# Optimization experiments

Measured on AMD Instinct MI355X. Metric: run time of the kernel, lower is better.

Reference implementation:

```python
import jax, jax.numpy as jnp
import numpy as np

IN_DIM, BANDS = 42, 22
H_VAD, H_NOISE, H_DEN = 24, 48, 96


def gru(x, w_ih, w_hh, b_ih, b_hh):
    """torch.nn.GRU (batch_first) semantics, h0=0.
    x: [B,T,D]; w_ih: [3H,D]; w_hh: [3H,H]; gate order r,z,n."""
    H = w_hh.shape[1]
    # precompute input projections for all timesteps (big GEMM, recurrence only on H)
    xp = jnp.einsum('btd,gd->btg', x, w_ih) + b_ih  # [B,T,3H]

    def step(h, xt):
        hp = h @ w_hh.T + b_hh
        xr, xz, xn = jnp.split(xt, 3, axis=-1)
        hr, hz, hn = jnp.split(hp, 3, axis=-1)
        r = jax.nn.sigmoid(xr + hr)
        z = jax.nn.sigmoid(xz + hz)
        n = jnp.tanh(xn + r * hn)
        h_new = (1.0 - z) * n + z * h
        return h_new, h_new

    h0 = jnp.zeros((x.shape[0], H), x.dtype)
    _, hs = jax.lax.scan(step, h0, jnp.swapaxes(xp, 0, 1))  # [T,B,H]
    return jnp.swapaxes(hs, 0, 1)  # [B,T,H]


def setup_inputs() -> dict:
    key = jax.random.key(0)
    ks = jax.random.split(key, 20)

    def w(k, shape, fan):
        return (jax.random.normal(k, shape, jnp.float32) / np.sqrt(fan)).astype(jnp.float32)

    B, T = 256, 2000
    d_noise_in = H_VAD + H_VAD + IN_DIM     # 90
    d_den_in = H_VAD + H_NOISE + IN_DIM     # 114
    return {
        'x': jax.random.normal(ks[0], (B, T, IN_DIM), jnp.float32),
        'in_w': w(ks[1], (H_VAD, IN_DIM), IN_DIM),
        'in_b': jnp.zeros((H_VAD,), jnp.float32),
        'vad_wih': w(ks[2], (3 * H_VAD, H_VAD), H_VAD),
        'vad_whh': w(ks[3], (3 * H_VAD, H_VAD), H_VAD),
        'vad_bih': jnp.zeros((3 * H_VAD,), jnp.float32),
        'vad_bhh': jnp.zeros((3 * H_VAD,), jnp.float32),
        'vad_out_w': w(ks[4], (1, H_VAD), H_VAD),
        'vad_out_b': jnp.zeros((1,), jnp.float32),
        'noise_wih': w(ks[5], (3 * H_NOISE, d_noise_in), d_noise_in),
        'noise_whh': w(ks[6], (3 * H_NOISE, H_NOISE), H_NOISE),
        'noise_bih': jnp.zeros((3 * H_NOISE,), jnp.float32),
        'noise_bhh': jnp.zeros((3 * H_NOISE,), jnp.float32),
        'den_wih': w(ks[7], (3 * H_DEN, d_den_in), d_den_in),
        'den_whh': w(ks[8], (3 * H_DEN, H_DEN), H_DEN),
        'den_bih': jnp.zeros((3 * H_DEN,), jnp.float32),
        'den_bhh': jnp.zeros((3 * H_DEN,), jnp.float32),
        'out_w': w(ks[9], (BANDS, H_DEN), H_DEN),
        'out_b': jnp.zeros((BANDS,), jnp.float32),
    }


def reference(x, in_w, in_b, vad_wih, vad_whh, vad_bih, vad_bhh,
              vad_out_w, vad_out_b, noise_wih, noise_whh, noise_bih, noise_bhh,
              den_wih, den_whh, den_bih, den_bhh, out_w, out_b):
    tmp = jnp.tanh(jnp.einsum('btd,hd->bth', x, in_w) + in_b)          # [B,T,24]
    vad_h = gru(tmp, vad_wih, vad_whh, vad_bih, vad_bhh)               # [B,T,24]
    vad = jax.nn.sigmoid(jnp.einsum('bth,oh->bto', vad_h, vad_out_w) + vad_out_b)
    noise_in = jnp.concatenate([tmp, vad_h, x], axis=-1)               # [B,T,90]
    noise_h = gru(noise_in, noise_wih, noise_whh, noise_bih, noise_bhh)  # [B,T,48]
    den_in = jnp.concatenate([vad_h, noise_h, x], axis=-1)             # [B,T,114]
    den_h = gru(den_in, den_wih, den_whh, den_bih, den_bhh)            # [B,T,96]
    gains = jax.nn.sigmoid(jnp.einsum('bth,oh->bto', den_h, out_w) + out_b)
    return gains, vad
```

## Files before the change

kernel.cpp:

```cpp
#include <hip/hip_runtime.h>

typedef _Float16 f16;
typedef _Float16 h2 __attribute__((ext_vector_type(2)));
typedef unsigned int u32;

#define TB  256
#define TTT 2000
#define INW 42
#define HV  24
#define HN  48
#define HD  96
#define NTH 640

#define DIN 0
#define DH  128
#define NIN 224
#define NH  320
#define ACTW 384

__device__ __forceinline__ float fsigm(float v) {
    return __builtin_amdgcn_rcpf(1.0f + __builtin_amdgcn_exp2f(-1.44269504089f * v));
}
__device__ __forceinline__ float ftanh(float v) {
    float e = __builtin_amdgcn_exp2f(2.88539008178f * v);
    return 1.0f - 2.0f * __builtin_amdgcn_rcpf(e + 1.0f);
}
__device__ __forceinline__ float dot2f(u32 a, u32 w, float c) {
#if __has_builtin(__builtin_amdgcn_fdot2)
    return __builtin_amdgcn_fdot2(__builtin_bit_cast(h2, a), __builtin_bit_cast(h2, w), c, false);
#else
    h2 av = __builtin_bit_cast(h2, a), wv = __builtin_bit_cast(h2, w);
    return c + (float)av[0] * (float)wv[0] + (float)av[1] * (float)wv[1];
#endif
}
__device__ __forceinline__ u32 packw(float a, float b) {
    h2 v; v[0] = (f16)a; v[1] = (f16)b;
    return __builtin_bit_cast(u32, v);
}
template<int CTRL>
__device__ __forceinline__ float dpp_add(float x) {
    int y = __builtin_amdgcn_mov_dpp(__builtin_bit_cast(int, x), CTRL, 0xF, 0xF, true);
    return x + __builtin_bit_cast(float, y);
}

#define SYNCB() asm volatile("s_waitcnt lgkmcnt(0)\n\ts_barrier" ::: "memory")

#define ACCI(AV, W, IDX) do { u32 _a = (AV); \
    rr = dot2f(_a, W[0][IDX], rr); zz = dot2f(_a, W[1][IDX], zz); an = dot2f(_a, W[2][IDX], an); } while (0)
#define ACCH(AV, W, IDX) do { u32 _a = (AV); \
    rr = dot2f(_a, W[0][IDX], rr); zz = dot2f(_a, W[1][IDX], zz); hn = dot2f(_a, W[2][IDX], hn); } while (0)
#define ACCI4(U4, W, M0) do { uint4 _u4 = (U4); \
    ACCI(_u4.x, W, (M0)+0); ACCI(_u4.y, W, (M0)+1); ACCI(_u4.z, W, (M0)+2); ACCI(_u4.w, W, (M0)+3); } while (0)
#define ACCH4(U4, W, M0) do { uint4 _u4 = (U4); \
    ACCH(_u4.x, W, (M0)+0); ACCH(_u4.y, W, (M0)+1); ACCH(_u4.z, W, (M0)+2); ACCH(_u4.w, W, (M0)+3); } while (0)
#define RED4_Q() do { \
    rr = dpp_add<0xB1>(rr); rr = dpp_add<0x4E>(rr); \
    zz = dpp_add<0xB1>(zz); zz = dpp_add<0x4E>(zz); \
    an = dpp_add<0xB1>(an); an = dpp_add<0x4E>(an); \
    hn = dpp_add<0xB1>(hn); hn = dpp_add<0x4E>(hn); } while (0)
#define RED4_1() do { \
    rr = dpp_add<0xB1>(rr); zz = dpp_add<0xB1>(zz); \
    an = dpp_add<0xB1>(an); hn = dpp_add<0xB1>(hn); } while (0)

template<int N> struct IC { static constexpr int val = N; };

__global__ __launch_bounds__(NTH, 1) void rnnoise_kernel(
    const float* __restrict__ gx,
    const float* __restrict__ in_w,      const float* __restrict__ in_b,
    const float* __restrict__ vad_wih,   const float* __restrict__ vad_whh,
    const float* __restrict__ vad_bih,   const float* __restrict__ vad_bhh,
    const float* __restrict__ vad_out_w, const float* __restrict__ vad_out_b,
    const float* __restrict__ noise_wih, const float* __restrict__ noise_whh,
    const float* __restrict__ noise_bih, const float* __restrict__ noise_bhh,
    const float* __restrict__ den_wih,   const float* __restrict__ den_whh,
    const float* __restrict__ den_bih,   const float* __restrict__ den_bhh,
    const float* __restrict__ out_w,     const float* __restrict__ out_b,
    float* __restrict__ gains, float* __restrict__ vout)
{
    __shared__ __align__(16) f16 act[8][ACTW];

    const int tid = threadIdx.x, wid = tid >> 6, lane = tid & 63;
    const int b = blockIdx.x;

    #pragma unroll
    for (int i = 0; i < 3; ++i) {
        int idx = tid + i * NTH;
        if (idx < 8 * ACTW / 2) ((u32*)act)[idx] = 0u;
    }
    __syncthreads();

    const int role = (wid == 9) ? 2 : ((wid == 4 || wid == 5 || wid == 8) ? 1 : 0);

    if (role == 0) {
        const int dwi = (wid < 4) ? wid : (wid - 2);
        const int u = 16 * dwi + (lane >> 2), q = lane & 3;
        u32 wdi[3][16], wdh[3][12];
        #pragma unroll
        for (int g = 0; g < 3; ++g) {
            const float* wi = den_wih + (g * HD + u) * 114;
            #pragma unroll
            for (int m = 0; m < 16; ++m) {
                int c = 32 * q + 2 * m;
                float a  = (c     < 114) ? wi[c]     : 0.f;
                float b2 = (c + 1 < 114) ? wi[c + 1] : 0.f;
                wdi[g][m] = packw(a, b2);
            }
            const float* wh = den_whh + (g * HD + u) * HD + 24 * q;
            #pragma unroll
            for (int m = 0; m < 12; ++m) wdh[g][m] = packw(wh[2*m], wh[2*m+1]);
        }
        const float bdr  = den_bih[u]        + den_bhh[u];
        const float bdz  = den_bih[HD + u]   + den_bhh[HD + u];
        const float bdni = den_bih[2*HD + u];
        const float bdnh = den_bhh[2*HD + u];
        float hreg = 0.f;
        float rr = 0.f, zz = 0.f, an = 0.f;

        auto step = [&](auto PC, int k) {
            constexpr int P   = decltype(PC)::val;
            constexpr int SHH = (P + 2) & 7;
            constexpr int SWR = (P + 3) & 7;
            constexpr int SB  = (P + 4) & 7;
            uint4 a0{}, a1{}, a2{}, a3{};
            if (k >= 4 && k < TTT + 4) {
                const uint4* ip = (const uint4*)&act[SB][DIN + 32 * q];
                a0 = ip[0]; a1 = ip[1]; a2 = ip[2]; a3 = ip[3];
            }
            if (k >= 5 && k < TTT + 5) {
                const uint4* hp = (const uint4*)&act[SHH][DH + 24 * q];
                uint4 h0 = hp[0], h1 = hp[1], h2 = hp[2];
                float hn = 0.f;
                ACCH4(h0, wdh, 0); ACCH4(h1, wdh, 4); ACCH4(h2, wdh, 8);
                RED4_Q();
                if (q == 0) {
                    float r = fsigm(rr + bdr);
                    float z = fsigm(zz + bdz);
                    float n = ftanh(an + bdni + r * (hn + bdnh));
                    hreg = z * (hreg - n) + n;
                    act[SWR][DH + u] = (f16)hreg;
                }
                rr = 0.f; zz = 0.f; an = 0.f;
            }
            if (k >= 4 && k < TTT + 4) {
                ACCI4(a0, wdi, 0); ACCI4(a1, wdi, 4); ACCI4(a2, wdi, 8); ACCI4(a3, wdi, 12);
            }
            SYNCB();
        };
        #pragma clang loop unroll(disable)
        for (int k0 = 0; k0 < TTT + 8; k0 += 8) {
            step(IC<0>{},k0);   step(IC<1>{},k0+1); step(IC<2>{},k0+2); step(IC<3>{},k0+3);
            step(IC<4>{},k0+4); step(IC<5>{},k0+5); step(IC<6>{},k0+6); step(IC<7>{},k0+7);
        }

    } else if (role == 1) {
        const int nwi = (wid == 4) ? 0 : ((wid == 5) ? 1 : 2);
        const int u = 16 * nwi + (lane >> 2), q = lane & 3;
        const int o = 8 * nwi + (lane >> 3), s8 = lane & 7;
        const int oc = (o < 22) ? o : 0;
        u32 wni[3][12], wnh[3][8], wo[6];
        #pragma unroll
        for (int g = 0; g < 3; ++g) {
            const float* wi = noise_wih + (g * HN + u) * 90;
            #pragma unroll
            for (int m = 0; m < 12; ++m) {
                int c = 24 * q + 2 * m;
                float a  = (c     < 90) ? wi[c]     : 0.f;
                float b2 = (c + 1 < 90) ? wi[c + 1] : 0.f;
                wni[g][m] = packw(a, b2);
            }
            const float* wh = noise_whh + (g * HN + u) * HN;
            #pragma unroll
            for (int m = 0; m < 8; ++m) {
                int c = 16 * q + 2 * m;
                float a  = (c     < 48) ? wh[c]     : 0.f;
                float b2 = (c + 1 < 48) ? wh[c + 1] : 0.f;
                wnh[g][m] = packw(a, b2);
            }
        }
        #pragma unroll
        for (int m = 0; m < 6; ++m)
            wo[m] = packw(out_w[oc*HD + 12*s8 + 2*m], out_w[oc*HD + 12*s8 + 2*m + 1]);
        const float bnr  = noise_bih[u]        + noise_bhh[u];
        const float bnz  = noise_bih[HN + u]   + noise_bhh[HN + u];
        const float bnni = noise_bih[2*HN + u];
        const float bnnh = noise_bhh[2*HN + u];
        const float bo   = out_b[oc];
        float hreg = 0.f;
        float rr = 0.f, zz = 0.f, an = 0.f;

        auto step = [&](auto PC, int k) {
            constexpr int P   = decltype(PC)::val;
            constexpr int SHH = (P + 4) & 7;
            constexpr int SWR = (P + 5) & 7;
            constexpr int SB  = (P + 6) & 7;
            constexpr int SOT = (P + 2) & 7;
            uint4 a0{}, a1{}, a2{};
            if (k >= 2 && k < TTT + 2) {
                const uint4* ip = (const uint4*)&act[SB][NIN + 24 * q];
                a0 = ip[0]; a1 = ip[1]; a2 = ip[2];
            }
            uint2 d0{}, d1{}, d2{};
            if (k >= 6 && k < TTT + 6) {
                const uint2* dp = (const uint2*)&act[SOT][DH + 12 * s8];
                d0 = dp[0]; d1 = dp[1]; d2 = dp[2];
            }
            if (k >= 3 && k < TTT + 3) {
                const uint4* hp = (const uint4*)&act[SHH][NH + 16 * q];
                uint4 h0 = hp[0], h1 = hp[1];
                float hn = 0.f;
                ACCH4(h0, wnh, 0); ACCH4(h1, wnh, 4);
                RED4_Q();
                if (q == 0) {
                    float r = fsigm(rr + bnr);
                    float z = fsigm(zz + bnz);
                    float n = ftanh(an + bnni + r * (hn + bnnh));
                    hreg = z * (hreg - n) + n;
                    f16 hh = (f16)hreg;
                    act[SWR][NH + u]       = hh;
                    act[SWR][DIN + 24 + u] = hh;
                }
                rr = 0.f; zz = 0.f; an = 0.f;
            }
            if (k >= 6 && k < TTT + 6) {
                float acc = 0;
                acc = dot2f(d0.x, wo[0], acc); acc = dot2f(d0.y, wo[1], acc);
                acc = dot2f(d1.x, wo[2], acc); acc = dot2f(d1.y, wo[3], acc);
                acc = dot2f(d2.x, wo[4], acc); acc = dot2f(d2.y, wo[5], acc);
                acc = dpp_add<0xB1>(acc); acc = dpp_add<0x4E>(acc);
                acc += __shfl_xor(acc, 4);
                if (s8 == 0 && o < 22)
                    gains[((size_t)b * TTT + (k - 6)) * 22 + o] = fsigm(acc + bo);
            }
            if (k >= 2 && k < TTT + 2) {
                ACCI4(a0, wni, 0); ACCI4(a1, wni, 4); ACCI4(a2, wni, 8);
            }
            SYNCB();
        };
        #pragma clang loop unroll(disable)
        for (int k0 = 0; k0 < TTT + 8; k0 += 8) {
            step(IC<0>{},k0);   step(IC<1>{},k0+1); step(IC<2>{},k0+2); step(IC<3>{},k0+3);
            step(IC<4>{},k0+4); step(IC<5>{},k0+5); step(IC<6>{},k0+6); step(IC<7>{},k0+7);
        }

    } else {
        const int l = lane;
        const int u = (l < 48) ? (l >> 1) : 0, q2 = l & 1;
        u32 wvi[3][6], wvh[3][6], wtm[12];
        float bvr = 0, bvz = 0, bvni = 0, bvnh = 0, btm = 0, wvo_u = 0;
        if (l < 48) {
            #pragma unroll
            for (int g = 0; g < 3; ++g) {
                const float* wi = vad_wih + (g * HV + u) * HV + 12 * q2;
                const float* wh = vad_whh + (g * HV + u) * HV + 12 * q2;
                #pragma unroll
                for (int j = 0; j < 6; ++j) {
                    wvi[g][j] = packw(wi[2*j], wi[2*j+1]);
                    wvh[g][j] = packw(wh[2*j], wh[2*j+1]);
                }
            }
            #pragma unroll
            for (int j = 0; j < 12; ++j) {
                int c0 = 24 * q2 + 2 * j;
                float a = (c0     < INW) ? in_w[u * INW + c0]     : 0.f;
                float c = (c0 + 1 < INW) ? in_w[u * INW + c0 + 1] : 0.f;
                wtm[j] = packw(a, c);
            }
            bvr  = vad_bih[u]        + vad_bhh[u];
            bvz  = vad_bih[HV + u]   + vad_bhh[HV + u];
            bvni = vad_bih[2*HV + u];
            bvnh = vad_bhh[2*HV + u];
            btm  = in_b[u];
            if (q2 == 0) wvo_u = vad_out_w[u];
        }
        const float bvo = vad_out_b[0];
        float hreg = 0.f;

        float xa = 0, xb = 0, xc = 0, xd = 0;
        if (l < INW) {
            xa = gx[((size_t)b * TTT + 0) * INW + l];
            xb = gx[((size_t)b * TTT + 1) * INW + l];
            xc = gx[((size_t)b * TTT + 2) * INW + l];
            xd = gx[((size_t)b * TTT + 3) * INW + l];
        }

        auto step = [&](auto PC, int k) {
            constexpr int P  = decltype(PC)::val;
            constexpr int ST = (P + 7) & 7;
            constexpr int SH = (P + 6) & 7;
            if (k < TTT && l < INW) {
                float xv;
                if constexpr ((P & 3) == 0) xv = xa; else if constexpr ((P & 3) == 1) xv = xb;
                else if constexpr ((P & 3) == 2) xv = xc; else xv = xd;
                f16 xh = (f16)xv;
                act[P][NIN + 48 + l] = xh;
                act[P][DIN + 72 + l] = xh;
            }
            if (k + 4 < TTT && l < INW) {
                float xv = gx[((size_t)b * TTT + (k + 4)) * INW + l];
                if constexpr ((P & 3) == 0) xa = xv; else if constexpr ((P & 3) == 1) xb = xv;
                else if constexpr ((P & 3) == 2) xc = xv; else xd = xv;
            }
            if (k >= 1 && k <= TTT) {
                float rr = 0, zz = 0, an = 0, hn = 0;
                if (l < 48) {
                    const uint2* tp = (const uint2*)&act[ST][NIN + 12 * q2];
                    const uint2* hp = (const uint2*)&act[SH][NIN + 24 + 12 * q2];
                    #pragma unroll
                    for (int v = 0; v < 3; ++v) {
                        uint2 a = tp[v]; ACCI(a.x, wvi, 2*v); ACCI(a.y, wvi, 2*v+1);
                        uint2 h = hp[v]; ACCH(h.x, wvh, 2*v); ACCH(h.y, wvh, 2*v+1);
                    }
                    RED4_1();
                    if (q2 == 0) {
                        float r = fsigm(rr + bvr);
                        float z = fsigm(zz + bvz);
                        float n = ftanh(an + bvni + r * (hn + bvnh));
                        hreg = z * (hreg - n) + n;
                        f16 hh = (f16)hreg;
                        act[ST][NIN + 24 + u] = hh;
                        act[ST][DIN + u]      = hh;
                    }
                }
                float val = (l < 48 && q2 == 0) ? (wvo_u * hreg) : 0.f;
                val = dpp_add<0xB1>(val);  val = dpp_add<0x4E>(val);
                val = dpp_add<0x124>(val); val = dpp_add<0x128>(val);
                val += __shfl_xor(val, 16); val += __shfl_xor(val, 32);
                if (l == 0) vout[(size_t)b * TTT + (k - 1)] = fsigm(val + bvo);
            }
            if (k < TTT && l < 48) {
                float acc = 0;
                const uint4* xp = (const uint4*)&act[P][NIN + 48 + 24 * q2];
                uint4 a = xp[0], b2 = xp[1], c2 = xp[2];
                acc = dot2f(a.x,  wtm[0], acc);  acc = dot2f(a.y,  wtm[1], acc);
                acc = dot2f(a.z,  wtm[2], acc);  acc = dot2f(a.w,  wtm[3], acc);
                acc = dot2f(b2.x, wtm[4], acc);  acc = dot2f(b2.y, wtm[5], acc);
                acc = dot2f(b2.z, wtm[6], acc);  acc = dot2f(b2.w, wtm[7], acc);
                acc = dot2f(c2.x, wtm[8], acc);  acc = dot2f(c2.y, wtm[9], acc);
                acc = dot2f(c2.z, wtm[10], acc); acc = dot2f(c2.w, wtm[11], acc);
                acc = dpp_add<0xB1>(acc);
                if (q2 == 0) act[P][NIN + u] = (f16)ftanh(acc + btm);
            }
            SYNCB();
        };
        #pragma clang loop unroll(disable)
        for (int k0 = 0; k0 < TTT + 8; k0 += 8) {
            step(IC<0>{},k0);   step(IC<1>{},k0+1); step(IC<2>{},k0+2); step(IC<3>{},k0+3);
            step(IC<4>{},k0+4); step(IC<5>{},k0+5); step(IC<6>{},k0+6); step(IC<7>{},k0+7);
        }
    }
}

extern "C" void kernel_launch(void* const* d_in, const int* in_sizes, int n_in,
                              void* d_out, int out_size, void* d_ws, size_t ws_size,
                              hipStream_t stream) {
    (void)in_sizes; (void)n_in; (void)d_ws; (void)ws_size; (void)out_size;
    const float* gx        = (const float*)d_in[0];
    const float* in_w      = (const float*)d_in[1];
    const float* in_b      = (const float*)d_in[2];
    const float* vad_wih   = (const float*)d_in[3];
    const float* vad_whh   = (const float*)d_in[4];
    const float* vad_bih   = (const float*)d_in[5];
    const float* vad_bhh   = (const float*)d_in[6];
    const float* vad_out_w = (const float*)d_in[7];
    const float* vad_out_b = (const float*)d_in[8];
    const float* noise_wih = (const float*)d_in[9];
    const float* noise_whh = (const float*)d_in[10];
    const float* noise_bih = (const float*)d_in[11];
    const float* noise_bhh = (const float*)d_in[12];
    const float* den_wih   = (const float*)d_in[13];
    const float* den_whh   = (const float*)d_in[14];
    const float* den_bih   = (const float*)d_in[15];
    const float* den_bhh   = (const float*)d_in[16];
    const float* out_w     = (const float*)d_in[17];
    const float* out_b     = (const float*)d_in[18];
    float* gains = (float*)d_out;
    float* vout  = (float*)d_out + (size_t)TB * (size_t)TTT * 22;

    rnnoise_kernel<<<dim3(TB), dim3(NTH), 0, stream>>>(
        gx, in_w, in_b, vad_wih, vad_whh, vad_bih, vad_bhh, vad_out_w, vad_out_b,
        noise_wih, noise_whh, noise_bih, noise_bhh, den_wih, den_whh, den_bih, den_bhh,
        out_w, out_b, gains, vout);
}
```

Before: 1.959 ms.

## Move gains output projection into denoise warps and software-pipeline input loads

Result: faster. 1.725 ms (-11.9%).

```diff
diff --git a/kernel.cpp b/kernel.cpp
--- a/kernel.cpp
+++ b/kernel.cpp
@@ -89,12 +89,15 @@
     }
     __syncthreads();
 
-    const int role = (wid == 9) ? 2 : ((wid == 4 || wid == 5 || wid == 8) ? 1 : 0);
+    const int role = (wid == 8) ? 2 : ((wid == 4 || wid == 5 || wid == 9) ? 1 : 0);
 
     if (role == 0) {
         const int dwi = (wid < 4) ? wid : (wid - 2);
         const int u = 16 * dwi + (lane >> 2), q = lane & 3;
-        u32 wdi[3][16], wdh[3][12];
+        const bool ow = (wid == 6 || wid == 7);
+        const int o = ((wid == 7) ? 11 : 0) + (lane >> 2);
+        const int oc = (ow && o < 22) ? o : 0;
+        u32 wdi[3][16], wdh[3][12], wo[12];
         #pragma unroll
         for (int g = 0; g < 3; ++g) {
             const float* wi = den_wih + (g * HD + u) * 114;
@@ -109,40 +112,50 @@
             #pragma unroll
             for (int m = 0; m < 12; ++m) wdh[g][m] = packw(wh[2*m], wh[2*m+1]);
         }
+        #pragma unroll
+        for (int m = 0; m < 12; ++m)
+            wo[m] = ow ? packw(out_w[oc*HD + 24*q + 2*m], out_w[oc*HD + 24*q + 2*m + 1]) : 0u;
         const float bdr  = den_bih[u]        + den_bhh[u];
         const float bdz  = den_bih[HD + u]   + den_bhh[HD + u];
         const float bdni = den_bih[2*HD + u];
         const float bdnh = den_bhh[2*HD + u];
+        const float bo   = ow ? out_b[oc] : 0.f;
         float hreg = 0.f;
-        float rr = 0.f, zz = 0.f, an = 0.f;
+        uint4 a0{}, a1{}, a2{}, a3{};
 
         auto step = [&](auto PC, int k) {
             constexpr int P   = decltype(PC)::val;
             constexpr int SHH = (P + 2) & 7;
             constexpr int SWR = (P + 3) & 7;
-            constexpr int SB  = (P + 4) & 7;
-            uint4 a0{}, a1{}, a2{}, a3{};
-            if (k >= 4 && k < TTT + 4) {
-                const uint4* ip = (const uint4*)&act[SB][DIN + 32 * q];
+            constexpr int SNX = (P + 4) & 7;
+            const uint4* hp = (const uint4*)&act[SHH][DH + 24 * q];
+            uint4 h0 = hp[0], h1 = hp[1], h2 = hp[2];
+            float rr = 0, zz = 0, an = 0, hn = 0;
+            ACCI4(a0, wdi, 0); ACCI4(a1, wdi, 4); ACCI4(a2, wdi, 8); ACCI4(a3, wdi, 12);
+            ACCH4(h0, wdh, 0); ACCH4(h1, wdh, 4); ACCH4(h2, wdh, 8);
+            RED4_Q();
+            if (k >= 5 && k < TTT + 5 && q == 0) {
+                float r = fsigm(rr + bdr);
+                float z = fsigm(zz + bdz);
+                float n = ftanh(an + bdni + r * (hn + bdnh));
+                hreg = z * (hreg - n) + n;
+                act[SWR][DH + u] = (f16)hreg;
+            }
+            {
+                const uint4* ip = (const uint4*)&act[SNX][DIN + 32 * q];
                 a0 = ip[0]; a1 = ip[1]; a2 = ip[2]; a3 = ip[3];
             }
-            if (k >= 5 && k < TTT + 5) {
-                const uint4* hp = (const uint4*)&act[SHH][DH + 24 * q];
-                uint4 h0 = hp[0], h1 = hp[1], h2 = hp[2];
-                float hn = 0.f;
-                ACCH4(h0, wdh, 0); ACCH4(h1, wdh, 4); ACCH4(h2, wdh, 8);
-                RED4_Q();
-                if (q == 0) {
-                    float r = fsigm(rr + bdr);
-                    float z = fsigm(zz + bdz);
-                    float n = ftanh(an + bdni + r * (hn + bdnh));
-                    hreg = z * (hreg - n) + n;
-                    act[SWR][DH + u] = (f16)hreg;
-                }
-                rr = 0.f; zz = 0.f; an = 0.f;
-            }
-            if (k >= 4 && k < TTT + 4) {
-                ACCI4(a0, wdi, 0); ACCI4(a1, wdi, 4); ACCI4(a2, wdi, 8); ACCI4(a3, wdi, 12);
+            if (ow && k >= 6 && k < TTT + 6) {
+                float acc = 0;
+                acc = dot2f(h0.x, wo[0], acc);  acc = dot2f(h0.y, wo[1], acc);
+                acc = dot2f(h0.z, wo[2], acc);  acc = dot2f(h0.w, wo[3], acc);
+                acc = dot2f(h1.x, wo[4], acc);  acc = dot2f(h1.y, wo[5], acc);
+                acc = dot2f(h1.z, wo[6], acc);  acc = dot2f(h1.w, wo[7], acc);
+                acc = dot2f(h2.x, wo[8], acc);  acc = dot2f(h2.y, wo[9], acc);
+                acc = dot2f(h2.z, wo[10], acc); acc = dot2f(h2.w, wo[11], acc);
+                acc = dpp_add<0xB1>(acc); acc = dpp_add<0x4E>(acc);
+                if (q == 0 && o < 22)
+                    gains[((size_t)b * TTT + (k - 6)) * 22 + o] = fsigm(acc + bo);
             }
             SYNCB();
         };
@@ -155,9 +168,7 @@
     } else if (role == 1) {
         const int nwi = (wid == 4) ? 0 : ((wid == 5) ? 1 : 2);
         const int u = 16 * nwi + (lane >> 2), q = lane & 3;
-        const int o = 8 * nwi + (lane >> 3), s8 = lane & 7;
-        const int oc = (o < 22) ? o : 0;
-        u32 wni[3][12], wnh[3][8], wo[6];
+        u32 wni[3][12], wnh[3][8];
         #pragma unroll
         for (int g = 0; g < 3; ++g) {
             const float* wi = noise_wih + (g * HN + u) * 90;
@@ -177,62 +188,36 @@
                 wnh[g][m] = packw(a, b2);
             }
         }
-        #pragma unroll
-        for (int m = 0; m < 6; ++m)
-            wo[m] = packw(out_w[oc*HD + 12*s8 + 2*m], out_w[oc*HD + 12*s8 + 2*m + 1]);
         const float bnr  = noise_bih[u]        + noise_bhh[u];
         const float bnz  = noise_bih[HN + u]   + noise_bhh[HN + u];
         const float bnni = noise_bih[2*HN + u];
         const float bnnh = noise_bhh[2*HN + u];
-        const float bo   = out_b[oc];
         float hreg = 0.f;
-        float rr = 0.f, zz = 0.f, an = 0.f;
+        uint4 a0{}, a1{}, a2{};
 
         auto step = [&](auto PC, int k) {
             constexpr int P   = decltype(PC)::val;
             constexpr int SHH = (P + 4) & 7;
             constexpr int SWR = (P + 5) & 7;
-            constexpr int SB  = (P + 6) & 7;
-            constexpr int SOT = (P + 2) & 7;
-            uint4 a0{}, a1{}, a2{};
-            if (k >= 2 && k < TTT + 2) {
-                const uint4* ip = (const uint4*)&act[SB][NIN + 24 * q];
+            constexpr int SNX = (P + 6) & 7;
+            const uint4* hp = (const uint4*)&act[SHH][NH + 16 * q];
+            uint4 h0 = hp[0], h1 = hp[1];
+            float rr = 0, zz = 0, an = 0, hn = 0;
+            ACCI4(a0, wni, 0); ACCI4(a1, wni, 4); ACCI4(a2, wni, 8);
+            ACCH4(h0, wnh, 0); ACCH4(h1, wnh, 4);
+            RED4_Q();
+            if (k >= 3 && k < TTT + 3 && q == 0) {
+                float r = fsigm(rr + bnr);
+                float z = fsigm(zz + bnz);
+                float n = ftanh(an + bnni + r * (hn + bnnh));
+                hreg = z * (hreg - n) + n;
+                f16 hh = (f16)hreg;
+                act[SWR][NH + u]       = hh;
+                act[SWR][DIN + 24 + u] = hh;
+            }
+            {
+                const uint4* ip = (const uint4*)&act[SNX][NIN + 24 * q];
                 a0 = ip[0]; a1 = ip[1]; a2 = ip[2];
-            }
-            uint2 d0{}, d1{}, d2{};
-            if (k >= 6 && k < TTT + 6) {
-                const uint2* dp = (const uint2*)&act[SOT][DH + 12 * s8];
-                d0 = dp[0]; d1 = dp[1]; d2 = dp[2];
-            }
-            if (k >= 3 && k < TTT + 3) {
-                const uint4* hp = (const uint4*)&act[SHH][NH + 16 * q];
-                uint4 h0 = hp[0], h1 = hp[1];
-                float hn = 0.f;
-                ACCH4(h0, wnh, 0); ACCH4(h1, wnh, 4);
-                RED4_Q();
-                if (q == 0) {
-                    float r = fsigm(rr + bnr);
-                    float z = fsigm(zz + bnz);
-                    float n = ftanh(an + bnni + r * (hn + bnnh));
-                    hreg = z * (hreg - n) + n;
-                    f16 hh = (f16)hreg;
-                    act[SWR][NH + u]       = hh;
-                    act[SWR][DIN + 24 + u] = hh;
-                }
-                rr = 0.f; zz = 0.f; an = 0.f;
-            }
-            if (k >= 6 && k < TTT + 6) {
-                float acc = 0;
-                acc = dot2f(d0.x, wo[0], acc); acc = dot2f(d0.y, wo[1], acc);
-                acc = dot2f(d1.x, wo[2], acc); acc = dot2f(d1.y, wo[3], acc);
-                acc = dot2f(d2.x, wo[4], acc); acc = dot2f(d2.y, wo[5], acc);
-                acc = dpp_add<0xB1>(acc); acc = dpp_add<0x4E>(acc);
-                acc += __shfl_xor(acc, 4);
-                if (s8 == 0 && o < 22)
-                    gains[((size_t)b * TTT + (k - 6)) * 22 + o] = fsigm(acc + bo);
-            }
-            if (k >= 2 && k < TTT + 2) {
-                ACCI4(a0, wni, 0); ACCI4(a1, wni, 4); ACCI4(a2, wni, 8);
             }
             SYNCB();
         };
```
